# Kernel optimization log

Measured on AMD Instinct MI355X. Metric: run time of the kernel, lower is better.

## Reference

```python
import jax, jax.numpy as jnp
import numpy as np

IN_CH = 64
HIDDEN_CH = 256

def setup_inputs() -> dict:
    key = jax.random.key(0)
    k = jax.random.split(key, 8)
    za = jax.random.normal(k[0], (8, 256, IN_CH), dtype=jnp.float32)
    zb = jax.random.normal(k[1], (8, 256, IN_CH), dtype=jnp.float32)
    # 1x1 conv weights stored as (out_ch, in_ch); biases zero per torch init
    w0 = jax.random.normal(k[2], (HIDDEN_CH, IN_CH), dtype=jnp.float32) * 0.05
    b0 = jnp.zeros((HIDDEN_CH,), dtype=jnp.float32)
    w1 = jax.random.normal(k[3], (HIDDEN_CH, HIDDEN_CH), dtype=jnp.float32) * 0.05
    b1 = jnp.zeros((HIDDEN_CH,), dtype=jnp.float32)
    w2 = jax.random.normal(k[4], (1, HIDDEN_CH), dtype=jnp.float32) * 0.05
    b2 = jnp.zeros((1,), dtype=jnp.float32)
    return {"za": za, "zb": zb, "w0": w0, "b0": b0, "w1": w1, "b1": b1, "w2": w2, "b2": b2}

def _leaky_relu(x):
    return jnp.where(x >= 0, x, 0.01 * x)  # torch LeakyReLU default slope

def reference(za, zb, w0, b0, w1, b1, w2, b2):
    # z_dif: (N, A, B, C) pairwise broadcast difference (channel-last; 1x1 conv = per-pixel linear)
    z_dif = za[:, :, None, :] - zb[:, None, :, :]
    y = _leaky_relu(jnp.einsum('nabc,hc->nabh', z_dif, w0) + b0)
    y = _leaky_relu(jnp.einsum('nabh,gh->nabg', y, w1) + b1)
    y = jax.nn.sigmoid(jnp.einsum('nabh,oh->nabo', y, w2) + b2)
    return y[..., 0]  # (N, A, B)
```

## Files before the change

kernel.cpp:

```cpp
#include <hip/hip_runtime.h>
#include <hip/hip_fp16.h>


typedef float f32x16 __attribute__((ext_vector_type(16)));
typedef _Float16 f16x8 __attribute__((ext_vector_type(8)));

__global__ __launch_bounds__(256) void pack_all(
    const float* __restrict__ za, const float* __restrict__ zb,
    const float* __restrict__ w0, const float* __restrict__ b0,
    const float* __restrict__ w1,
    _Float16* __restrict__ upack, _Float16* __restrict__ vpack,
    _Float16* __restrict__ w1pk) {
  int bid = blockIdx.x;
  int tid = threadIdx.x;
  if (bid < 2048) {
    int nr = bid;
    int n = nr >> 8, r = nr & 255;
    __shared__ float arow[64], brow[64];
    if (tid < 64) arow[tid] = za[nr * 64 + tid];
    else if (tid < 128) brow[tid - 64] = zb[nr * 64 + (tid - 64)];
    __syncthreads();
    int h = tid;
    const float* w0r = w0 + h * 64;
    float ua = 0.f, vb = 0.f;
#pragma unroll
    for (int c = 0; c < 64; c += 4) {
      float4 w = *reinterpret_cast<const float4*>(w0r + c);
      ua += w.x * arow[c] + w.y * arow[c + 1] + w.z * arow[c + 2] + w.w * arow[c + 3];
      vb += w.x * brow[c] + w.y * brow[c + 1] + w.z * brow[c + 2] + w.w * brow[c + 3];
    }
    upack[nr * 256 + h] = (_Float16)(ua + b0[h]);
    int bblk = r >> 5, lcol = r & 31;
    int kiter = h >> 4, rem = h & 15, lh = rem >> 3, j = rem & 7;
    int lane = lh * 32 + lcol;
    vpack[(((n * 8 + bblk) * 16 + kiter) * 64 + lane) * 8 + j] = (_Float16)vb;
  } else {
    int id = (bid - 2048) * 256 + tid;
    int g = id >> 8, k = id & 255;
    int gt = g >> 5, lcol = g & 31;
    int kiter = k >> 4, rem = k & 15, lh = rem >> 3, j = rem & 7;
    int lane = lh * 32 + lcol;
    w1pk[((kiter * 8 + gt) * 64 + lane) * 8 + j] = (_Float16)w1[id];
  }
}

__global__ __launch_bounds__(512, 2) void fused_main(
    const _Float16* __restrict__ upack, const _Float16* __restrict__ vpack,
    const _Float16* __restrict__ w1pk,
    const float* __restrict__ b1, const float* __restrict__ w2,
    const float* __restrict__ b2, float* __restrict__ out) {
  __shared__ float lds_p[2][8][32];
  int bid = blockIdx.x;
  int n = bid >> 5;
  int bblk = (bid >> 2) & 7;
  int aq = bid & 3;
  int tid = threadIdx.x;
  int ws = tid >> 6;
  int l = tid & 63;
  int l31 = l & 31, lh = l >> 5;

  f16x8 w1f[16];
#pragma unroll
  for (int kt = 0; kt < 16; ++kt)
    w1f[kt] = *reinterpret_cast<const f16x8*>(w1pk + ((kt * 8 + ws) * 64 + l) * 8);

  float b1f[16], w2f[16];
#pragma unroll
  for (int rg = 0; rg < 4; ++rg) {
    int gbase = ws * 32 + 8 * rg + 4 * lh;
    float4 bb = *reinterpret_cast<const float4*>(b1 + gbase);
    float4 ww = *reinterpret_cast<const float4*>(w2 + gbase);
    b1f[4 * rg + 0] = bb.x; b1f[4 * rg + 1] = bb.y;
    b1f[4 * rg + 2] = bb.z; b1f[4 * rg + 3] = bb.w;
    w2f[4 * rg + 0] = ww.x; w2f[4 * rg + 1] = ww.y;
    w2f[4 * rg + 2] = ww.z; w2f[4 * rg + 3] = ww.w;
  }
  float b2v = b2[0];

  const _Float16 c001 = (_Float16)0.01f;
  const f16x8 c001v = {c001, c001, c001, c001, c001, c001, c001, c001};

  const _Float16* vb = vpack + (size_t)((n * 8 + bblk) * 16) * 512 + l * 8;
  const _Float16* ub = upack + (size_t)(n * 256 + aq * 64) * 256 + lh * 8;

  for (int it = 0; it < 64; ++it) {
    const _Float16* ur = ub + (size_t)it * 256;

    f32x16 accA, accB;
#pragma unroll
    for (int r = 0; r < 16; ++r) { accA[r] = 0.f; accB[r] = 0.f; }

#pragma unroll
    for (int kt = 0; kt < 16; ++kt) {
      f16x8 uu = *reinterpret_cast<const f16x8*>(ur + kt * 16);
      f16x8 vv = *reinterpret_cast<const f16x8*>(vb + kt * 512);
      f16x8 d = uu - vv;
      f16x8 r = __builtin_elementwise_max(d, d * c001v);
      if (kt & 1)
        accB = __builtin_amdgcn_mfma_f32_32x32x16_f16(w1f[kt], r, accB, 0, 0, 0);
      else
        accA = __builtin_amdgcn_mfma_f32_32x32x16_f16(w1f[kt], r, accA, 0, 0, 0);
    }

    float p = 0.f;
#pragma unroll
    for (int r = 0; r < 16; ++r) {
      float h = accA[r] + accB[r] + b1f[r];
      h = fmaxf(h, 0.01f * h);
      p = fmaf(h, w2f[r], p);
    }
    p += __shfl_xor(p, 32, 64);

    int ph = it & 1;
    if (l < 32) lds_p[ph][ws][l] = p;
    __syncthreads();
    if (ws == 0 && l < 32) {
      float s = b2v;
#pragma unroll
      for (int w = 0; w < 8; ++w) s += lds_p[ph][w][l];
      int a = aq * 64 + it;
      out[(size_t)(n * 256 + a) * 256 + bblk * 32 + l] = 1.f / (1.f + __expf(-s));
    }
  }
}

extern "C" void kernel_launch(void* const* d_in, const int* in_sizes, int n_in,
                              void* d_out, int out_size, void* d_ws, size_t ws_size,
                              hipStream_t stream) {
  const float* za = (const float*)d_in[0];
  const float* zb = (const float*)d_in[1];
  const float* w0 = (const float*)d_in[2];
  const float* b0 = (const float*)d_in[3];
  const float* w1 = (const float*)d_in[4];
  const float* b1 = (const float*)d_in[5];
  const float* w2 = (const float*)d_in[6];
  const float* b2 = (const float*)d_in[7];
  float* out = (float*)d_out;

  char* ws = (char*)d_ws;
  _Float16* upack = (_Float16*)ws;
  _Float16* vpack = (_Float16*)(ws + (1u << 20));
  _Float16* w1pk  = (_Float16*)(ws + (2u << 20));

  pack_all<<<2304, 256, 0, stream>>>(za, zb, w0, b0, w1, upack, vpack, w1pk);
  fused_main<<<256, 512, 0, stream>>>(upack, vpack, w1pk, b1, w2, b2, out);
}
```

Baseline: 158.3 us.

## Split LeakyReLU into linear and abs parts, precompute linear term per row

Rewrites the first LeakyReLU as 0.505*x + 0.495*|x| and folds the 0.495 factor into the packed W1. The linear part W1*(u-v) is precomputed per row by a new kernel into Ra (with b1) and Sb and used to initialize the accumulators. The inner loop then only needs an abs via bitmask instead of a multiply and max. The v fragments are also hoisted into registers. This adds a launch, extra workspace traffic and per-iteration fp32 loads of Ra in exchange for fewer VALU ops in the hot loop.

```diff
diff --git a/kernel.cpp b/kernel.cpp
--- a/kernel.cpp
+++ b/kernel.cpp
@@ -4,13 +4,14 @@
 
 typedef float f32x16 __attribute__((ext_vector_type(16)));
 typedef _Float16 f16x8 __attribute__((ext_vector_type(8)));
+typedef int i32x4 __attribute__((ext_vector_type(4)));
 
 __global__ __launch_bounds__(256) void pack_all(
     const float* __restrict__ za, const float* __restrict__ zb,
     const float* __restrict__ w0, const float* __restrict__ b0,
     const float* __restrict__ w1,
     _Float16* __restrict__ upack, _Float16* __restrict__ vpack,
-    _Float16* __restrict__ w1pk) {
+    _Float16* __restrict__ vlin, _Float16* __restrict__ w1pk) {
   int bid = blockIdx.x;
   int tid = threadIdx.x;
   if (bid < 2048) {
@@ -30,25 +31,67 @@
       vb += w.x * brow[c] + w.y * brow[c + 1] + w.z * brow[c + 2] + w.w * brow[c + 3];
     }
     upack[nr * 256 + h] = (_Float16)(ua + b0[h]);
+    _Float16 vh = (_Float16)vb;
+    vlin[nr * 256 + h] = vh;
     int bblk = r >> 5, lcol = r & 31;
     int kiter = h >> 4, rem = h & 15, lh = rem >> 3, j = rem & 7;
     int lane = lh * 32 + lcol;
-    vpack[(((n * 8 + bblk) * 16 + kiter) * 64 + lane) * 8 + j] = (_Float16)vb;
+    vpack[(((n * 8 + bblk) * 16 + kiter) * 64 + lane) * 8 + j] = vh;
   } else {
     int id = (bid - 2048) * 256 + tid;
     int g = id >> 8, k = id & 255;
     int gt = g >> 5, lcol = g & 31;
     int kiter = k >> 4, rem = k & 15, lh = rem >> 3, j = rem & 7;
     int lane = lh * 32 + lcol;
-    w1pk[((kiter * 8 + gt) * 64 + lane) * 8 + j] = (_Float16)w1[id];
+    w1pk[((kiter * 8 + gt) * 64 + lane) * 8 + j] = (_Float16)(0.495f * w1[id]);
+  }
+}
+
+__global__ __launch_bounds__(256) void pq_kernel(
+    const _Float16* __restrict__ upack, const _Float16* __restrict__ vlin,
+    const float* __restrict__ w1, const float* __restrict__ b1,
+    float* __restrict__ Ra, float* __restrict__ Sb) {
+  int bid = blockIdx.x;
+  int which = bid >> 9;
+  int nr0 = (bid & 511) * 4;
+  __shared__ float rows[4][256];
+  int tid = threadIdx.x;
+  const _Float16* src = which ? vlin : upack;
+#pragma unroll
+  for (int i = 0; i < 4; ++i)
+    rows[i][tid] = (float)src[(size_t)(nr0 + i) * 256 + tid];
+  __syncthreads();
+  int g = tid;
+  const float* w1r = w1 + (size_t)g * 256;
+  float acc0 = 0.f, acc1 = 0.f, acc2 = 0.f, acc3 = 0.f;
+#pragma unroll 8
+  for (int k = 0; k < 256; k += 4) {
+    float4 w = *reinterpret_cast<const float4*>(w1r + k);
+    acc0 += w.x * rows[0][k] + w.y * rows[0][k + 1] + w.z * rows[0][k + 2] + w.w * rows[0][k + 3];
+    acc1 += w.x * rows[1][k] + w.y * rows[1][k + 1] + w.z * rows[1][k + 2] + w.w * rows[1][k + 3];
+    acc2 += w.x * rows[2][k] + w.y * rows[2][k + 1] + w.z * rows[2][k + 2] + w.w * rows[2][k + 3];
+    acc3 += w.x * rows[3][k] + w.y * rows[3][k + 1] + w.z * rows[3][k + 2] + w.w * rows[3][k + 3];
+  }
+  if (which == 0) {
+    float bb = b1[g];
+    Ra[(size_t)(nr0 + 0) * 256 + g] = 0.505f * acc0 + bb;
+    Ra[(size_t)(nr0 + 1) * 256 + g] = 0.505f * acc1 + bb;
+    Ra[(size_t)(nr0 + 2) * 256 + g] = 0.505f * acc2 + bb;
+    Ra[(size_t)(nr0 + 3) * 256 + g] = 0.505f * acc3 + bb;
+  } else {
+    Sb[(size_t)(nr0 + 0) * 256 + g] = 0.505f * acc0;
+    Sb[(size_t)(nr0 + 1) * 256 + g] = 0.505f * acc1;
+    Sb[(size_t)(nr0 + 2) * 256 + g] = 0.505f * acc2;
+    Sb[(size_t)(nr0 + 3) * 256 + g] = 0.505f * acc3;
   }
 }
 
 __global__ __launch_bounds__(512, 2) void fused_main(
     const _Float16* __restrict__ upack, const _Float16* __restrict__ vpack,
     const _Float16* __restrict__ w1pk,
-    const float* __restrict__ b1, const float* __restrict__ w2,
-    const float* __restrict__ b2, float* __restrict__ out) {
+    const float* __restrict__ Ra, const float* __restrict__ Sb,
+    const float* __restrict__ w2, const float* __restrict__ b2,
+    float* __restrict__ out) {
   __shared__ float lds_p[2][8][32];
   int bid = blockIdx.x;
   int n = bid >> 5;
@@ -64,49 +107,63 @@
   for (int kt = 0; kt < 16; ++kt)
     w1f[kt] = *reinterpret_cast<const f16x8*>(w1pk + ((kt * 8 + ws) * 64 + l) * 8);
 
-  float b1f[16], w2f[16];
+  const _Float16* vbase = vpack + (size_t)((n * 8 + bblk) * 16) * 512 + l * 8;
+  f16x8 vf[16];
+#pragma unroll
+  for (int kt = 0; kt < 16; ++kt)
+    vf[kt] = *reinterpret_cast<const f16x8*>(vbase + kt * 512);
+
+  float sbf[16], w2f[16];
+  const float* sbrow = Sb + (size_t)(n * 256 + bblk * 32 + l31) * 256;
 #pragma unroll
   for (int rg = 0; rg < 4; ++rg) {
     int gbase = ws * 32 + 8 * rg + 4 * lh;
-    float4 bb = *reinterpret_cast<const float4*>(b1 + gbase);
+    float4 ss = *reinterpret_cast<const float4*>(sbrow + gbase);
     float4 ww = *reinterpret_cast<const float4*>(w2 + gbase);
-    b1f[4 * rg + 0] = bb.x; b1f[4 * rg + 1] = bb.y;
-    b1f[4 * rg + 2] = bb.z; b1f[4 * rg + 3] = bb.w;
+    sbf[4 * rg + 0] = ss.x; sbf[4 * rg + 1] = ss.y;
+    sbf[4 * rg + 2] = ss.z; sbf[4 * rg + 3] = ss.w;
     w2f[4 * rg + 0] = ww.x; w2f[4 * rg + 1] = ww.y;
     w2f[4 * rg + 2] = ww.z; w2f[4 * rg + 3] = ww.w;
   }
   float b2v = b2[0];
 
-  const _Float16 c001 = (_Float16)0.01f;
-  const f16x8 c001v = {c001, c001, c001, c001, c001, c001, c001, c001};
-
-  const _Float16* vb = vpack + (size_t)((n * 8 + bblk) * 16) * 512 + l * 8;
   const _Float16* ub = upack + (size_t)(n * 256 + aq * 64) * 256 + lh * 8;
+  const float* rabase = Ra + (size_t)(n * 256 + aq * 64) * 256;
 
   for (int it = 0; it < 64; ++it) {
     const _Float16* ur = ub + (size_t)it * 256;
+    const float* rar = rabase + (size_t)it * 256;
 
     f32x16 accA, accB;
 #pragma unroll
-    for (int r = 0; r < 16; ++r) { accA[r] = 0.f; accB[r] = 0.f; }
+    for (int rg = 0; rg < 4; ++rg) {
+      float4 rr = *reinterpret_cast<const float4*>(rar + ws * 32 + 8 * rg + 4 * lh);
+      accA[4 * rg + 0] = rr.x - sbf[4 * rg + 0];
+      accA[4 * rg + 1] = rr.y - sbf[4 * rg + 1];
+      accA[4 * rg + 2] = rr.z - sbf[4 * rg + 2];
+      accA[4 * rg + 3] = rr.w - sbf[4 * rg + 3];
+    }
+#pragma unroll
+    for (int r = 0; r < 16; ++r) accB[r] = 0.f;
 
 #pragma unroll
     for (int kt = 0; kt < 16; ++kt) {
       f16x8 uu = *reinterpret_cast<const f16x8*>(ur + kt * 16);
-      f16x8 vv = *reinterpret_cast<const f16x8*>(vb + kt * 512);
-      f16x8 d = uu - vv;
-      f16x8 r = __builtin_elementwise_max(d, d * c001v);
+      f16x8 d = uu - vf[kt];
+      i32x4 di = __builtin_bit_cast(i32x4, d);
+      di &= 0x7fff7fff;
+      f16x8 ad = __builtin_bit_cast(f16x8, di);
       if (kt & 1)
-        accB = __builtin_amdgcn_mfma_f32_32x32x16_f16(w1f[kt], r, accB, 0, 0, 0);
+        accB = __builtin_amdgcn_mfma_f32_32x32x16_f16(w1f[kt], ad, accB, 0, 0, 0);
       else
-        accA = __builtin_amdgcn_mfma_f32_32x32x16_f16(w1f[kt], r, accA, 0, 0, 0);
+        accA = __builtin_amdgcn_mfma_f32_32x32x16_f16(w1f[kt], ad, accA, 0, 0, 0);
     }
 
     float p = 0.f;
 #pragma unroll
     for (int r = 0; r < 16; ++r) {
-      float h = accA[r] + accB[r] + b1f[r];
-      h = fmaxf(h, 0.01f * h);
+      float s = accA[r] + accB[r];
+      float h = fmaxf(s, 0.01f * s);
       p = fmaf(h, w2f[r], p);
     }
     p += __shfl_xor(p, 32, 64);
@@ -140,8 +197,12 @@
   char* ws = (char*)d_ws;
   _Float16* upack = (_Float16*)ws;
   _Float16* vpack = (_Float16*)(ws + (1u << 20));
-  _Float16* w1pk  = (_Float16*)(ws + (2u << 20));
-
-  pack_all<<<2304, 256, 0, stream>>>(za, zb, w0, b0, w1, upack, vpack, w1pk);
-  fused_main<<<256, 512, 0, stream>>>(upack, vpack, w1pk, b1, w2, b2, out);
-}
+  _Float16* vlin  = (_Float16*)(ws + (2u << 20));
+  _Float16* w1pk  = (_Float16*)(ws + (3u << 20));
+  float*    Ra    = (float*)(ws + (7u << 19));
+  float*    Sb    = (float*)(ws + (11u << 19));
+
+  pack_all<<<2304, 256, 0, stream>>>(za, zb, w0, b0, w1, upack, vpack, vlin, w1pk);
+  pq_kernel<<<1024, 256, 0, stream>>>(upack, vlin, w1, b1, Ra, Sb);
+  fused_main<<<256, 512, 0, stream>>>(upack, vpack, w1pk, Ra, Sb, w2, b2, out);
+}
```

After: 196.0 us. 1.24x slower.
